# Performance work log

Hardware: AMD Instinct MI355X
Metric: run time of the kernel (lower is better)

The kernel has to match this reference:

```python
import jax, jax.numpy as jnp
import numpy as np

NEG_BIG = -9e15
ALPHA = 0.2  # LeakyReLU negative slope
B, N, F_IN, F_OUT = 8, 2048, 128, 128


def setup_inputs() -> dict:
    key = jax.random.key(0)
    k1, k2, k3, k4 = jax.random.split(key, 4)
    inp = jax.random.normal(k1, (B, N, F_IN), dtype=jnp.float32)
    adj = jax.random.randint(k2, (B, N, N), 0, 2, dtype=jnp.int32)
    W = 0.02 * jax.random.normal(k3, (F_OUT, F_IN), dtype=jnp.float32)  # nn.Linear weight [out,in]
    a = 0.02 * jax.random.normal(k4, (1, 2 * F_OUT), dtype=jnp.float32)  # attention vector [1, 2F]
    return {"input": inp, "adj": adj, "W": W, "a": a}


def reference(input, adj, W, a):
    # h = input @ W^T : [B, N, F_OUT]
    h = jnp.einsum("bnf,of->bno", input, W)
    f_out = h.shape[-1]
    # Decompose a . [h_i || h_j] = (h_i . a1) + (h_j . a2) -- same math as the
    # explicit repeat_interleave/repeat/cat, without the O(N^2 * 2F) tensor.
    a1 = a[0, :f_out]
    a2 = a[0, f_out:]
    s1 = h @ a1  # [B, N] score for source node i
    s2 = h @ a2  # [B, N] score for target node j
    e = jax.nn.leaky_relu(s1[:, :, None] + s2[:, None, :], negative_slope=ALPHA)  # [B,N,N]
    masked = jnp.where(adj > 0, e, NEG_BIG)
    attention = jax.nn.softmax(masked, axis=-1)
    # dropout p=0.0 (eval) -> identity
    h_prime = jnp.einsum("bnm,bmo->bno", attention, h)
    return h_prime
```

## Files before the change

### kernel.cpp

```cpp
#include <hip/hip_runtime.h>
#include <stdint.h>


#define B_ 8
#define N_ 2048
#define FD 128
#define ALPHA_ 0.2f
#define TJ 64
#define NCHL 16
#define CHUNK_U4 1024

typedef __attribute__((ext_vector_type(8))) short short8;
typedef __attribute__((ext_vector_type(4))) float f32x4;

#define HCHUNK(o, jc) ((((o) * 16) + ((jc) ^ ((o) & 15))) * 8)
#define HC64(o, jc) ((o) * 8 + ((jc) ^ ((o) & 7)))

__device__ __forceinline__ float bf2f(unsigned short u) {
    union { uint32_t i; float f; } v; v.i = ((uint32_t)u) << 16; return v.f;
}
__device__ __forceinline__ unsigned short f2bf(float f) {
    union { float f; uint32_t i; } v; v.f = f;
    uint32_t x = v.i;
    uint32_t r = (x + 0x7fffu + ((x >> 16) & 1u)) >> 16;
    return (unsigned short)r;
}

__device__ __forceinline__ void gl2lds16(const uint4* g, uint4* l) {
    __builtin_amdgcn_global_load_lds(
        (const __attribute__((address_space(1))) uint32_t*)g,
        (__attribute__((address_space(3))) uint32_t*)l, 16, 0, 0);
}

__global__ __launch_bounds__(256) void gat_h(
    const float* __restrict__ x,
    const float* __restrict__ W,
    const float* __restrict__ a,
    unsigned short* __restrict__ hT,
    float* __restrict__ s1o, float* __restrict__ s2o)
{
    __shared__ __align__(16) unsigned short Wlds[FD * FD];

    const int bid = blockIdx.x;
    const int tid = threadIdx.x;
    const int w = tid >> 6;
    const int lane = tid & 63;
    const int m = lane & 15;
    const int quad = lane >> 4;
    const int arow = bid * 64 + w * 16 + m;

#pragma unroll
    for (int it = 0; it < 8; it++) {
        int cid = it * 256 + tid;
        int o = cid >> 4, kc = cid & 15;
        const float* wp = W + (size_t)o * FD + kc * 8;
        float4 w0 = *(const float4*)wp;
        float4 w1 = *(const float4*)(wp + 4);
        uint4 pk;
        pk.x = (uint32_t)f2bf(w0.x) | ((uint32_t)f2bf(w0.y) << 16);
        pk.y = (uint32_t)f2bf(w0.z) | ((uint32_t)f2bf(w0.w) << 16);
        pk.z = (uint32_t)f2bf(w1.x) | ((uint32_t)f2bf(w1.y) << 16);
        pk.w = (uint32_t)f2bf(w1.z) | ((uint32_t)f2bf(w1.w) << 16);
        *(uint4*)&Wlds[HCHUNK(o, kc)] = pk;
    }
    __syncthreads();

    f32x4 acc[8];
#pragma unroll
    for (int ot = 0; ot < 8; ot++) acc[ot] = (f32x4){0.f, 0.f, 0.f, 0.f};

#pragma unroll
    for (int ks = 0; ks < 4; ks++) {
        const float* xp = x + (size_t)arow * FD + ks * 32 + quad * 8;
        float4 x0 = *(const float4*)xp;
        float4 x1 = *(const float4*)(xp + 4);
        float xv[8] = {x0.x, x0.y, x0.z, x0.w, x1.x, x1.y, x1.z, x1.w};
        union { unsigned short us[8]; short8 v; } ahi, alo;
#pragma unroll
        for (int jj = 0; jj < 8; jj++) {
            unsigned short hi = f2bf(xv[jj]);
            ahi.us[jj] = hi;
            alo.us[jj] = f2bf(xv[jj] - bf2f(hi));
        }
#pragma unroll
        for (int ot = 0; ot < 8; ot++) {
            union { uint4 u; short8 v; } bw;
            bw.u = *(const uint4*)&Wlds[HCHUNK(ot * 16 + m, ks * 4 + quad)];
            acc[ot] = __builtin_amdgcn_mfma_f32_16x16x32_bf16(ahi.v, bw.v, acc[ot], 0, 0, 0);
            acc[ot] = __builtin_amdgcn_mfma_f32_16x16x32_bf16(alo.v, bw.v, acc[ot], 0, 0, 0);
        }
    }

    const int rc0 = bid * 64 + w * 16 + quad * 4;
    const int bb = rc0 >> 11;
    const int jb = rc0 & (N_ - 1);
    const int kc = jb >> 6;
    const int jcl = (jb & 63) >> 3;
    const int off = jb & 7;
    unsigned short* hTb = hT + (size_t)bb * FD * N_ + (size_t)kc * (CHUNK_U4 * 8);
    float s1p[4] = {0.f, 0.f, 0.f, 0.f};
    float s2p[4] = {0.f, 0.f, 0.f, 0.f};
#pragma unroll
    for (int ot = 0; ot < 8; ot++) {
        const int o = ot * 16 + m;
        uint2 pk;
        pk.x = (uint32_t)f2bf(acc[ot][0]) | ((uint32_t)f2bf(acc[ot][1]) << 16);
        pk.y = (uint32_t)f2bf(acc[ot][2]) | ((uint32_t)f2bf(acc[ot][3]) << 16);
        *(uint2*)(hTb + (size_t)HC64(o, jcl) * 8 + off) = pk;
        float a1v = a[o], a2v = a[FD + o];
#pragma unroll
        for (int r = 0; r < 4; r++) {
            s1p[r] += acc[ot][r] * a1v;
            s2p[r] += acc[ot][r] * a2v;
        }
    }
#pragma unroll
    for (int offx = 8; offx >= 1; offx >>= 1) {
#pragma unroll
        for (int r = 0; r < 4; r++) {
            s1p[r] += __shfl_xor(s1p[r], offx);
            s2p[r] += __shfl_xor(s2p[r], offx);
        }
    }
    if (m == 0) {
#pragma unroll
        for (int r = 0; r < 4; r++) {
            s1o[rc0 + r] = s1p[r];
            s2o[rc0 + r] = s2p[r];
        }
    }
}

__global__ __launch_bounds__(512, 2) void gat_attn(
    const int* __restrict__ adj,
    const unsigned short* __restrict__ hT,
    const float* __restrict__ s1,
    const float* __restrict__ s2,
    float* __restrict__ out)
{
    __shared__ __align__(16) uint4 hbuf[2][2][CHUNK_U4];
    __shared__ float rsx[4][16];

    const int bid = blockIdx.x;
    const int b = bid & 7;
    const int ib = bid >> 3;
    const int i0 = ib * 64;
    const int tid = threadIdx.x;
    const int lane = tid & 63;
    const int w = tid >> 6;
    const int jh = w & 1;
    const int rh = w >> 1;
    const int m = lane & 15;
    const int quad = lane >> 4;

    const int irow = i0 + rh * 16 + m;
    const float s1v = s1[b * N_ + irow];
    const int* adjrow = adj + ((size_t)(b * N_ + irow)) * N_ + jh * 1024;
    const uint4* hTc = (const uint4*)(hT + (size_t)b * FD * N_)
                       + (size_t)jh * NCHL * CHUNK_U4;
    const float* s2b = s2 + b * N_ + jh * 1024;

#pragma unroll
    for (int q = 0; q < 4; q++)
        gl2lds16(&hTc[(rh * 4 + q) * 64 + lane], &hbuf[jh][0][(rh * 4 + q) * 64]);
    int4 acur[4];
    float4 scur[4];
#pragma unroll
    for (int ks = 0; ks < 2; ks++) {
        acur[2 * ks]     = *(const int4*)(adjrow + ks * 32 + quad * 8);
        acur[2 * ks + 1] = *(const int4*)(adjrow + ks * 32 + quad * 8 + 4);
        scur[2 * ks]     = *(const float4*)(s2b + ks * 32 + quad * 8);
        scur[2 * ks + 1] = *(const float4*)(s2b + ks * 32 + quad * 8 + 4);
    }
    __syncthreads();

    f32x4 acc[8];
#pragma unroll
    for (int ot = 0; ot < 8; ot++) acc[ot] = (f32x4){0.f, 0.f, 0.f, 0.f};
    float rs_loc = 0.f;

    for (int k = 0; k < NCHL; k++) {
        const int buf = k & 1;
        const bool more = (k + 1 < NCHL);
        int4 anext[4];
        float4 snext[4];
        if (more) {
#pragma unroll
            for (int q = 0; q < 4; q++)
                gl2lds16(&hTc[(size_t)(k + 1) * CHUNK_U4 + (rh * 4 + q) * 64 + lane],
                         &hbuf[jh][buf ^ 1][(rh * 4 + q) * 64]);
            const int j1 = (k + 1) * TJ;
#pragma unroll
            for (int ks = 0; ks < 2; ks++) {
                anext[2 * ks]     = *(const int4*)(adjrow + j1 + ks * 32 + quad * 8);
                anext[2 * ks + 1] = *(const int4*)(adjrow + j1 + ks * 32 + quad * 8 + 4);
                snext[2 * ks]     = *(const float4*)(s2b + j1 + ks * 32 + quad * 8);
                snext[2 * ks + 1] = *(const float4*)(s2b + j1 + ks * 32 + quad * 8 + 4);
            }
        }

#pragma unroll
        for (int ks = 0; ks < 2; ks++) {
            float4 sa = scur[2 * ks], sb = scur[2 * ks + 1];
            float sarr[8] = {sa.x, sa.y, sa.z, sa.w, sb.x, sb.y, sb.z, sb.w};
            int4 A0 = acur[2 * ks], A1 = acur[2 * ks + 1];
            int aarr[8] = {A0.x, A0.y, A0.z, A0.w, A1.x, A1.y, A1.z, A1.w};
            union { unsigned short us[8]; short8 v; } af;
#pragma unroll
            for (int jj = 0; jj < 8; jj++) {
                float e = s1v + sarr[jj];
                e = (e > 0.f) ? e : (ALPHA_ * e);
                float p = (aarr[jj] > 0) ? __expf(e) : 0.f;
                rs_loc += p;
                af.us[jj] = f2bf(p);
            }
            const int jc = ks * 4 + quad;
#pragma unroll
            for (int ot = 0; ot < 8; ot++) {
                const int o = ot * 16 + m;
                union { uint4 u; short8 v; } bf;
                bf.u = *(const uint4*)&hbuf[jh][buf][HC64(o, jc)];
                acc[ot] = __builtin_amdgcn_mfma_f32_16x16x32_bf16(af.v, bf.v, acc[ot], 0, 0, 0);
            }
        }

        __syncthreads();
        if (more) {
#pragma unroll
            for (int q = 0; q < 4; q++) { acur[q] = anext[q]; scur[q] = snext[q]; }
        }
    }

    rs_loc += __shfl_xor(rs_loc, 16);
    rs_loc += __shfl_xor(rs_loc, 32);

    float* xch = (float*)&hbuf[0][0][0];
    if (jh == 1) {
#pragma unroll
        for (int ot = 0; ot < 8; ot++)
#pragma unroll
            for (int r = 0; r < 4; r++)
                xch[(rh * 16 + quad * 4 + r) * 130 + ot * 16 + m] = acc[ot][r];
        if (quad == 0) rsx[rh][m] = rs_loc;
    }
    __syncthreads();
    if (jh == 0) {
        float rinv[4];
#pragma unroll
        for (int r = 0; r < 4; r++) {
            const int p = quad * 4 + r;
            rinv[r] = 1.0f / (__shfl(rs_loc, p) + rsx[rh][p]);
        }
        float* outp = out + (size_t)(b * N_ + i0 + rh * 16) * FD;
#pragma unroll
        for (int ot = 0; ot < 8; ot++) {
            const int col = ot * 16 + m;
#pragma unroll
            for (int r = 0; r < 4; r++) {
                float v = acc[ot][r] + xch[(rh * 16 + quad * 4 + r) * 130 + col];
                outp[(size_t)(quad * 4 + r) * FD + col] = v * rinv[r];
            }
        }
    }
}

extern "C" void kernel_launch(void* const* d_in, const int* in_sizes, int n_in,
                              void* d_out, int out_size, void* d_ws, size_t ws_size,
                              hipStream_t stream) {
    const void* xv = d_in[0];
    const void* adjv = d_in[1];
    const void* Wv = d_in[2];
    const void* av = d_in[3];
    for (int i = 0; i < n_in; i++) {
        switch (in_sizes[i]) {
            case 2097152:  xv = d_in[i]; break;
            case 33554432: adjv = d_in[i]; break;
            case 16384:    Wv = d_in[i]; break;
            case 256:      av = d_in[i]; break;
            default: break;
        }
    }
    const float* x = (const float*)xv;
    const int* adj = (const int*)adjv;
    const float* W = (const float*)Wv;
    const float* a = (const float*)av;
    float* out = (float*)d_out;

    char* p = (char*)d_ws;
    unsigned short* hT = (unsigned short*)p;  p += (size_t)B_ * FD * N_ * 2;
    float* s1 = (float*)p;                    p += (size_t)B_ * N_ * 4;
    float* s2 = (float*)p;

    gat_h<<<256, 256, 0, stream>>>(x, W, a, hT, s1, s2);
    gat_attn<<<256, 512, 0, stream>>>(adj, hT, s1, s2, out);
}
```

Measured before the change: 222.7 us.

## Deepen LDS pipeline to 4 buffers with one barrier per chunk and counted waits

Expands the shared-memory h buffer from double to quadruple buffering and issues async global-to-LDS loads two chunks ahead. The per-iteration __syncthreads is replaced by a single s_barrier preceded by a partial vmcnt wait, so adjacency and score prefetches for the next chunk stay in flight. The main loop is fully unrolled via a macro with ping-pong register sets. This aims to hide global load latency and cut barrier stalls, at the cost of double the LDS footprint (which may hurt occupancy with 2 blocks per CU) and reliance on a hand-chosen vmcnt count.

```diff
diff --git a/kernel.cpp b/kernel.cpp
--- a/kernel.cpp
+++ b/kernel.cpp
@@ -131,6 +131,8 @@
     }
 }
 
+struct RegSet { int4 a[4]; float4 s[4]; };
+
 __global__ __launch_bounds__(512, 2) void gat_attn(
     const int* __restrict__ adj,
     const unsigned short* __restrict__ hT,
@@ -138,7 +140,7 @@
     const float* __restrict__ s2,
     float* __restrict__ out)
 {
-    __shared__ __align__(16) uint4 hbuf[2][2][CHUNK_U4];
+    __shared__ __align__(16) uint4 hbuf[2][4][CHUNK_U4];
     __shared__ float rsx[4][16];
 
     const int bid = blockIdx.x;
@@ -160,76 +162,97 @@
                        + (size_t)jh * NCHL * CHUNK_U4;
     const float* s2b = s2 + b * N_ + jh * 1024;
 
+    f32x4 acc[8];
+#pragma unroll
+    for (int ot = 0; ot < 8; ot++) acc[ot] = (f32x4){0.f, 0.f, 0.f, 0.f};
+    float rs_loc = 0.f;
+
+    RegSet RA, RB;
+
 #pragma unroll
     for (int q = 0; q < 4; q++)
         gl2lds16(&hTc[(rh * 4 + q) * 64 + lane], &hbuf[jh][0][(rh * 4 + q) * 64]);
-    int4 acur[4];
-    float4 scur[4];
+    asm volatile("" ::: "memory");
 #pragma unroll
     for (int ks = 0; ks < 2; ks++) {
-        acur[2 * ks]     = *(const int4*)(adjrow + ks * 32 + quad * 8);
-        acur[2 * ks + 1] = *(const int4*)(adjrow + ks * 32 + quad * 8 + 4);
-        scur[2 * ks]     = *(const float4*)(s2b + ks * 32 + quad * 8);
-        scur[2 * ks + 1] = *(const float4*)(s2b + ks * 32 + quad * 8 + 4);
-    }
-    __syncthreads();
-
-    f32x4 acc[8];
-#pragma unroll
-    for (int ot = 0; ot < 8; ot++) acc[ot] = (f32x4){0.f, 0.f, 0.f, 0.f};
-    float rs_loc = 0.f;
-
-    for (int k = 0; k < NCHL; k++) {
-        const int buf = k & 1;
-        const bool more = (k + 1 < NCHL);
-        int4 anext[4];
-        float4 snext[4];
-        if (more) {
-#pragma unroll
-            for (int q = 0; q < 4; q++)
-                gl2lds16(&hTc[(size_t)(k + 1) * CHUNK_U4 + (rh * 4 + q) * 64 + lane],
-                         &hbuf[jh][buf ^ 1][(rh * 4 + q) * 64]);
-            const int j1 = (k + 1) * TJ;
-#pragma unroll
-            for (int ks = 0; ks < 2; ks++) {
-                anext[2 * ks]     = *(const int4*)(adjrow + j1 + ks * 32 + quad * 8);
-                anext[2 * ks + 1] = *(const int4*)(adjrow + j1 + ks * 32 + quad * 8 + 4);
-                snext[2 * ks]     = *(const float4*)(s2b + j1 + ks * 32 + quad * 8);
-                snext[2 * ks + 1] = *(const float4*)(s2b + j1 + ks * 32 + quad * 8 + 4);
-            }
-        }
-
-#pragma unroll
-        for (int ks = 0; ks < 2; ks++) {
-            float4 sa = scur[2 * ks], sb = scur[2 * ks + 1];
-            float sarr[8] = {sa.x, sa.y, sa.z, sa.w, sb.x, sb.y, sb.z, sb.w};
-            int4 A0 = acur[2 * ks], A1 = acur[2 * ks + 1];
-            int aarr[8] = {A0.x, A0.y, A0.z, A0.w, A1.x, A1.y, A1.z, A1.w};
-            union { unsigned short us[8]; short8 v; } af;
-#pragma unroll
-            for (int jj = 0; jj < 8; jj++) {
-                float e = s1v + sarr[jj];
-                e = (e > 0.f) ? e : (ALPHA_ * e);
-                float p = (aarr[jj] > 0) ? __expf(e) : 0.f;
-                rs_loc += p;
-                af.us[jj] = f2bf(p);
-            }
-            const int jc = ks * 4 + quad;
-#pragma unroll
-            for (int ot = 0; ot < 8; ot++) {
-                const int o = ot * 16 + m;
-                union { uint4 u; short8 v; } bf;
-                bf.u = *(const uint4*)&hbuf[jh][buf][HC64(o, jc)];
-                acc[ot] = __builtin_amdgcn_mfma_f32_16x16x32_bf16(af.v, bf.v, acc[ot], 0, 0, 0);
-            }
-        }
-
-        __syncthreads();
-        if (more) {
-#pragma unroll
-            for (int q = 0; q < 4; q++) { acur[q] = anext[q]; scur[q] = snext[q]; }
-        }
-    }
+        RA.a[2 * ks]     = *(const int4*)(adjrow + ks * 32 + quad * 8);
+        RA.a[2 * ks + 1] = *(const int4*)(adjrow + ks * 32 + quad * 8 + 4);
+        RA.s[2 * ks]     = *(const float4*)(s2b + ks * 32 + quad * 8);
+        RA.s[2 * ks + 1] = *(const float4*)(s2b + ks * 32 + quad * 8 + 4);
+    }
+#pragma unroll
+    for (int q = 0; q < 4; q++)
+        gl2lds16(&hTc[(size_t)CHUNK_U4 + (rh * 4 + q) * 64 + lane],
+                 &hbuf[jh][1][(rh * 4 + q) * 64]);
+
+#define GAT_ITER(K, RC, RN)                                                    \
+    {                                                                          \
+        if ((K) + 1 < NCHL) {                                                  \
+            const int j1 = ((K) + 1) * TJ;                                     \
+            RN.a[0] = *(const int4*)(adjrow + j1 + quad * 8);                  \
+            RN.a[1] = *(const int4*)(adjrow + j1 + quad * 8 + 4);              \
+            RN.a[2] = *(const int4*)(adjrow + j1 + 32 + quad * 8);             \
+            RN.a[3] = *(const int4*)(adjrow + j1 + 32 + quad * 8 + 4);         \
+            RN.s[0] = *(const float4*)(s2b + j1 + quad * 8);                   \
+            RN.s[1] = *(const float4*)(s2b + j1 + quad * 8 + 4);               \
+            RN.s[2] = *(const float4*)(s2b + j1 + 32 + quad * 8);              \
+            RN.s[3] = *(const float4*)(s2b + j1 + 32 + quad * 8 + 4);          \
+        }                                                                      \
+        if ((K) < NCHL - 1) asm volatile("s_waitcnt vmcnt(12)" ::: "memory");  \
+        else                asm volatile("s_waitcnt vmcnt(0)" ::: "memory");   \
+        __builtin_amdgcn_s_barrier();                                          \
+        asm volatile("" ::: "memory");                                         \
+        if ((K) + 2 < NCHL) {                                                  \
+            _Pragma("unroll")                                                  \
+            for (int q = 0; q < 4; q++)                                        \
+                gl2lds16(&hTc[(size_t)((K) + 2) * CHUNK_U4 + (rh * 4 + q) * 64 \
+                              + lane],                                         \
+                         &hbuf[jh][((K) + 2) & 3][(rh * 4 + q) * 64]);         \
+        }                                                                      \
+        _Pragma("unroll")                                                      \
+        for (int ks = 0; ks < 2; ks++) {                                       \
+            float4 sa = RC.s[2 * ks], sb = RC.s[2 * ks + 1];                   \
+            float sarr[8] = {sa.x, sa.y, sa.z, sa.w, sb.x, sb.y, sb.z, sb.w};  \
+            int4 A0 = RC.a[2 * ks], A1 = RC.a[2 * ks + 1];                     \
+            int aarr[8] = {A0.x, A0.y, A0.z, A0.w, A1.x, A1.y, A1.z, A1.w};    \
+            union { unsigned short us[8]; short8 v; } af;                      \
+            _Pragma("unroll")                                                  \
+            for (int jj = 0; jj < 8; jj++) {                                   \
+                float e = s1v + sarr[jj];                                      \
+                e = (e > 0.f) ? e : (ALPHA_ * e);                              \
+                float p = (aarr[jj] > 0) ? __expf(e) : 0.f;                    \
+                rs_loc += p;                                                   \
+                af.us[jj] = f2bf(p);                                           \
+            }                                                                  \
+            const int jc = ks * 4 + quad;                                      \
+            _Pragma("unroll")                                                  \
+            for (int ot = 0; ot < 8; ot++) {                                   \
+                const int o = ot * 16 + m;                                     \
+                union { uint4 u; short8 v; } bf;                               \
+                bf.u = *(const uint4*)&hbuf[jh][(K) & 3][HC64(o, jc)];         \
+                acc[ot] = __builtin_amdgcn_mfma_f32_16x16x32_bf16(             \
+                    af.v, bf.v, acc[ot], 0, 0, 0);                             \
+            }                                                                  \
+        }                                                                      \
+    }
+
+    GAT_ITER(0,  RA, RB)
+    GAT_ITER(1,  RB, RA)
+    GAT_ITER(2,  RA, RB)
+    GAT_ITER(3,  RB, RA)
+    GAT_ITER(4,  RA, RB)
+    GAT_ITER(5,  RB, RA)
+    GAT_ITER(6,  RA, RB)
+    GAT_ITER(7,  RB, RA)
+    GAT_ITER(8,  RA, RB)
+    GAT_ITER(9,  RB, RA)
+    GAT_ITER(10, RA, RB)
+    GAT_ITER(11, RB, RA)
+    GAT_ITER(12, RA, RB)
+    GAT_ITER(13, RB, RA)
+    GAT_ITER(14, RA, RB)
+    GAT_ITER(15, RB, RA)
+#undef GAT_ITER
 
     rs_loc += __shfl_xor(rs_loc, 16);
     rs_loc += __shfl_xor(rs_loc, 32);
```

New measurement: 254.2 us. 14.1% more time.

## Split attention over four j-quarters with 32-row blocks and 32-wide chunks

Applied to the files above, without the earlier changes.

Each attention block now covers 32 query rows instead of 64, with four wave pairs that each handle a quarter of the key range. Chunks shrink to 32 keys, and the hT layout and swizzle are changed to match. The grid doubles to 512 blocks and launch bounds ask for 4 blocks per CU, aiming for more occupancy and more parallelism while streaming the adjacency matrix. The cost is a larger cross-wave reduction of partial outputs and row sums through LDS, plus less reuse of each hT chunk per row.

```diff
diff --git a/kernel.cpp b/kernel.cpp
--- a/kernel.cpp
+++ b/kernel.cpp
@@ -6,15 +6,15 @@
 #define N_ 2048
 #define FD 128
 #define ALPHA_ 0.2f
-#define TJ 64
-#define NCHL 16
-#define CHUNK_U4 1024
+#define TJ 32
+#define NCH 16
+#define CHU4 512
 
 typedef __attribute__((ext_vector_type(8))) short short8;
 typedef __attribute__((ext_vector_type(4))) float f32x4;
 
 #define HCHUNK(o, jc) ((((o) * 16) + ((jc) ^ ((o) & 15))) * 8)
-#define HC64(o, jc) ((o) * 8 + ((jc) ^ ((o) & 7)))
+#define U32(o, jc) (((o) >> 1) * 8 + ((((((o) & 1) << 2)) | (jc)) ^ (((o) >> 1) & 7)))
 
 __device__ __forceinline__ float bf2f(unsigned short u) {
     union { uint32_t i; float f; } v; v.i = ((uint32_t)u) << 16; return v.f;
@@ -94,10 +94,10 @@
     const int rc0 = bid * 64 + w * 16 + quad * 4;
     const int bb = rc0 >> 11;
     const int jb = rc0 & (N_ - 1);
-    const int kc = jb >> 6;
-    const int jcl = (jb & 63) >> 3;
+    const int kc = jb >> 5;
+    const int jc2 = (jb & 31) >> 3;
     const int off = jb & 7;
-    unsigned short* hTb = hT + (size_t)bb * FD * N_ + (size_t)kc * (CHUNK_U4 * 8);
+    unsigned short* hTb = hT + (size_t)bb * FD * N_ + (size_t)kc * (CHU4 * 8);
     float s1p[4] = {0.f, 0.f, 0.f, 0.f};
     float s2p[4] = {0.f, 0.f, 0.f, 0.f};
 #pragma unroll
@@ -106,7 +106,7 @@
         uint2 pk;
         pk.x = (uint32_t)f2bf(acc[ot][0]) | ((uint32_t)f2bf(acc[ot][1]) << 16);
         pk.y = (uint32_t)f2bf(acc[ot][2]) | ((uint32_t)f2bf(acc[ot][3]) << 16);
-        *(uint2*)(hTb + (size_t)HC64(o, jcl) * 8 + off) = pk;
+        *(uint2*)(hTb + (size_t)U32(o, jc2) * 8 + off) = pk;
         float a1v = a[o], a2v = a[FD + o];
 #pragma unroll
         for (int r = 0; r < 4; r++) {
@@ -131,47 +131,42 @@
     }
 }
 
-__global__ __launch_bounds__(512, 2) void gat_attn(
+__global__ __launch_bounds__(512, 4) void gat_attn(
     const int* __restrict__ adj,
     const unsigned short* __restrict__ hT,
     const float* __restrict__ s1,
     const float* __restrict__ s2,
     float* __restrict__ out)
 {
-    __shared__ __align__(16) uint4 hbuf[2][2][CHUNK_U4];
-    __shared__ float rsx[4][16];
+    __shared__ __align__(16) uint4 hbuf[4][2][CHU4];
+    __shared__ float rsq[4][2][16];
 
     const int bid = blockIdx.x;
     const int b = bid & 7;
     const int ib = bid >> 3;
-    const int i0 = ib * 64;
+    const int i0 = ib * 32;
     const int tid = threadIdx.x;
     const int lane = tid & 63;
     const int w = tid >> 6;
-    const int jh = w & 1;
-    const int rh = w >> 1;
+    const int rh = w & 1;
+    const int jq = w >> 1;
     const int m = lane & 15;
     const int quad = lane >> 4;
 
     const int irow = i0 + rh * 16 + m;
     const float s1v = s1[b * N_ + irow];
-    const int* adjrow = adj + ((size_t)(b * N_ + irow)) * N_ + jh * 1024;
-    const uint4* hTc = (const uint4*)(hT + (size_t)b * FD * N_)
-                       + (size_t)jh * NCHL * CHUNK_U4;
-    const float* s2b = s2 + b * N_ + jh * 1024;
+    const int* adjrow = adj + ((size_t)(b * N_ + irow)) * N_ + jq * 512;
+    const float* s2q = s2 + b * N_ + jq * 512;
+    const uint4* hTq = (const uint4*)hT + (size_t)b * (FD * N_ / 8)
+                       + (size_t)jq * NCH * CHU4;
 
 #pragma unroll
     for (int q = 0; q < 4; q++)
-        gl2lds16(&hTc[(rh * 4 + q) * 64 + lane], &hbuf[jh][0][(rh * 4 + q) * 64]);
-    int4 acur[4];
-    float4 scur[4];
-#pragma unroll
-    for (int ks = 0; ks < 2; ks++) {
-        acur[2 * ks]     = *(const int4*)(adjrow + ks * 32 + quad * 8);
-        acur[2 * ks + 1] = *(const int4*)(adjrow + ks * 32 + quad * 8 + 4);
-        scur[2 * ks]     = *(const float4*)(s2b + ks * 32 + quad * 8);
-        scur[2 * ks + 1] = *(const float4*)(s2b + ks * 32 + quad * 8 + 4);
-    }
+        gl2lds16(&hTq[rh * 256 + q * 64 + lane], &hbuf[jq][0][rh * 256 + q * 64]);
+    int4 a0 = *(const int4*)(adjrow + quad * 8);
+    int4 a1 = *(const int4*)(adjrow + quad * 8 + 4);
+    float4 sc0 = *(const float4*)(s2q + quad * 8);
+    float4 sc1 = *(const float4*)(s2q + quad * 8 + 4);
     __syncthreads();
 
     f32x4 acc[8];
@@ -179,32 +174,26 @@
     for (int ot = 0; ot < 8; ot++) acc[ot] = (f32x4){0.f, 0.f, 0.f, 0.f};
     float rs_loc = 0.f;
 
-    for (int k = 0; k < NCHL; k++) {
+    for (int k = 0; k < NCH; k++) {
         const int buf = k & 1;
-        const bool more = (k + 1 < NCHL);
-        int4 anext[4];
-        float4 snext[4];
+        const bool more = (k + 1 < NCH);
+        int4 na0, na1;
+        float4 ns0, ns1;
         if (more) {
 #pragma unroll
             for (int q = 0; q < 4; q++)
-                gl2lds16(&hTc[(size_t)(k + 1) * CHUNK_U4 + (rh * 4 + q) * 64 + lane],
-                         &hbuf[jh][buf ^ 1][(rh * 4 + q) * 64]);
+                gl2lds16(&hTq[(size_t)(k + 1) * CHU4 + rh * 256 + q * 64 + lane],
+                         &hbuf[jq][buf ^ 1][rh * 256 + q * 64]);
             const int j1 = (k + 1) * TJ;
-#pragma unroll
-            for (int ks = 0; ks < 2; ks++) {
-                anext[2 * ks]     = *(const int4*)(adjrow + j1 + ks * 32 + quad * 8);
-                anext[2 * ks + 1] = *(const int4*)(adjrow + j1 + ks * 32 + quad * 8 + 4);
-                snext[2 * ks]     = *(const float4*)(s2b + j1 + ks * 32 + quad * 8);
-                snext[2 * ks + 1] = *(const float4*)(s2b + j1 + ks * 32 + quad * 8 + 4);
-            }
-        }
-
-#pragma unroll
-        for (int ks = 0; ks < 2; ks++) {
-            float4 sa = scur[2 * ks], sb = scur[2 * ks + 1];
-            float sarr[8] = {sa.x, sa.y, sa.z, sa.w, sb.x, sb.y, sb.z, sb.w};
-            int4 A0 = acur[2 * ks], A1 = acur[2 * ks + 1];
-            int aarr[8] = {A0.x, A0.y, A0.z, A0.w, A1.x, A1.y, A1.z, A1.w};
+            na0 = *(const int4*)(adjrow + j1 + quad * 8);
+            na1 = *(const int4*)(adjrow + j1 + quad * 8 + 4);
+            ns0 = *(const float4*)(s2q + j1 + quad * 8);
+            ns1 = *(const float4*)(s2q + j1 + quad * 8 + 4);
+        }
+
+        {
+            float sarr[8] = {sc0.x, sc0.y, sc0.z, sc0.w, sc1.x, sc1.y, sc1.z, sc1.w};
+            int aarr[8] = {a0.x, a0.y, a0.z, a0.w, a1.x, a1.y, a1.z, a1.w};
             union { unsigned short us[8]; short8 v; } af;
 #pragma unroll
             for (int jj = 0; jj < 8; jj++) {
@@ -214,42 +203,41 @@
                 rs_loc += p;
                 af.us[jj] = f2bf(p);
             }
-            const int jc = ks * 4 + quad;
 #pragma unroll
             for (int ot = 0; ot < 8; ot++) {
                 const int o = ot * 16 + m;
                 union { uint4 u; short8 v; } bf;
-                bf.u = *(const uint4*)&hbuf[jh][buf][HC64(o, jc)];
+                bf.u = *(const uint4*)&hbuf[jq][buf][U32(o, quad)];
                 acc[ot] = __builtin_amdgcn_mfma_f32_16x16x32_bf16(af.v, bf.v, acc[ot], 0, 0, 0);
             }
         }
 
         __syncthreads();
-        if (more) {
-#pragma unroll
-            for (int q = 0; q < 4; q++) { acur[q] = anext[q]; scur[q] = snext[q]; }
-        }
+        if (more) { a0 = na0; a1 = na1; sc0 = ns0; sc1 = ns1; }
     }
 
     rs_loc += __shfl_xor(rs_loc, 16);
     rs_loc += __shfl_xor(rs_loc, 32);
 
     float* xch = (float*)&hbuf[0][0][0];
-    if (jh == 1) {
+    if (jq != 0) {
 #pragma unroll
         for (int ot = 0; ot < 8; ot++)
 #pragma unroll
             for (int r = 0; r < 4; r++)
-                xch[(rh * 16 + quad * 4 + r) * 130 + ot * 16 + m] = acc[ot][r];
-        if (quad == 0) rsx[rh][m] = rs_loc;
+                xch[((jq - 1) * 32 + rh * 16 + quad * 4 + r) * 132 + ot * 16 + m]
+                    = acc[ot][r];
+        if (quad == 0) rsq[jq][rh][m] = rs_loc;
     }
     __syncthreads();
-    if (jh == 0) {
+    if (jq == 0) {
         float rinv[4];
 #pragma unroll
         for (int r = 0; r < 4; r++) {
             const int p = quad * 4 + r;
-            rinv[r] = 1.0f / (__shfl(rs_loc, p) + rsx[rh][p]);
+            float rtot = __shfl(rs_loc, p)
+                       + rsq[1][rh][p] + rsq[2][rh][p] + rsq[3][rh][p];
+            rinv[r] = 1.0f / rtot;
         }
         float* outp = out + (size_t)(b * N_ + i0 + rh * 16) * FD;
 #pragma unroll
@@ -257,7 +245,11 @@
             const int col = ot * 16 + m;
 #pragma unroll
             for (int r = 0; r < 4; r++) {
-                float v = acc[ot][r] + xch[(rh * 16 + quad * 4 + r) * 130 + col];
+                const int row = rh * 16 + quad * 4 + r;
+                float v = acc[ot][r]
+                        + xch[(row) * 132 + col]
+                        + xch[(32 + row) * 132 + col]
+                        + xch[(64 + row) * 132 + col];
                 outp[(size_t)(quad * 4 + r) * FD + col] = v * rinv[r];
             }
         }
@@ -292,5 +284,5 @@
     float* s2 = (float*)p;
 
     gat_h<<<256, 256, 0, stream>>>(x, W, a, hT, s1, s2);
-    gat_attn<<<256, 512, 0, stream>>>(adj, hT, s1, s2, out);
-}
+    gat_attn<<<512, 512, 0, stream>>>(adj, hT, s1, s2, out);
+}
```

Result: faster. 216.2 us (-2.9%).
